# Optimization experiments

Measured on AMD Instinct MI355X. Metric: run time of the kernel, lower is better.

## Reference

```python
import jax, jax.numpy as jnp
import numpy as np

IN_FEATURES = 4096
OUT_FEATURES = 11008
BATCH = 256


def unpack_i4(q):
    # q: [K//2, N] packed bytes; row 2k = low nibble, row 2k+1 = high nibble
    low = q & 15
    high = (q >> 4) & 15
    # interleave -> [K, N]
    return jnp.stack([low, high], axis=1).reshape(q.shape[0] * 2, q.shape[1])


def setup_inputs() -> dict:
    key = jax.random.key(0)
    k1, k2, k3, k4 = jax.random.split(key, 4)
    x = jax.random.normal(k1, (BATCH, IN_FEATURES), dtype=jnp.float32)
    qweight = jax.random.randint(k2, (IN_FEATURES // 2, OUT_FEATURES), 0, 256, dtype=jnp.int32)
    scales = jax.random.uniform(k3, (OUT_FEATURES,), dtype=jnp.float32)
    zeroes = jax.random.normal(k4, (OUT_FEATURES,), dtype=jnp.float32)
    return {"x": x, "qweight": qweight, "scales": scales, "zeroes": zeroes}


def reference(x, qweight, scales, zeroes):
    # Dequantize: per-output-channel scale/zero over unpacked int4 weights
    w = scales[None, :] * unpack_i4(qweight).astype(jnp.float32) - zeroes[None, :]  # [K, N]
    return x @ w  # [B, N]
```

## Files before the change

### kernel.cpp

```cpp
#include <hip/hip_runtime.h>
#include <stdint.h>

#define K_DIM 4096
#define N_DIM 11008
#define M_DIM 256

typedef uint32_t u32;
using frag_ab = __attribute__((ext_vector_type(8))) short;
using frag_cd = __attribute__((ext_vector_type(4))) float;

typedef __attribute__((address_space(3))) const char lds_cc;

#define DSR128(dst, addr, off)                                       \
    asm volatile("ds_read_b128 %0, %1 offset:" #off                  \
                 : "=&v"(dst) : "v"(addr))
#define DSR32(dst, addr, off)                                        \
    asm volatile("ds_read_b32 %0, %1 offset:" #off                   \
                 : "=&v"(dst) : "v"(addr))

__device__ __forceinline__ u32 f2bf_rn(float f) {
    u32 u = __builtin_bit_cast(u32, f);
    return (u + 0x7FFFu + ((u >> 16) & 1u)) >> 16;
}
__device__ __forceinline__ float bf2f(u32 b) {
    return __builtin_bit_cast(float, b << 16);
}
__device__ __forceinline__ void gll16(const void* g, void* l) {
    __builtin_amdgcn_global_load_lds(
        (const __attribute__((address_space(1))) u32*)g,
        (__attribute__((address_space(3))) u32*)l, 16, 0, 0);
}

#define BFCVT(q) ((u32)((__mul24((int)(q), 0x4004) & 0x003C003C) | 0x42004200))

__global__ __launch_bounds__(256) void prep_kernel(const float* __restrict__ x,
                                                   ushort* __restrict__ xbf,
                                                   float* __restrict__ rowsum) {
    const int row = blockIdx.x;
    const int tid = threadIdx.x;
    const float* xr = x + (size_t)row * K_DIM;
    ushort* br = xbf + (size_t)row * K_DIM;
    float s = 0.0f;
#pragma unroll
    for (int p = 0; p < 4; ++p) {
        int i = p * 1024 + tid * 4;
        float4 v = *reinterpret_cast<const float4*>(xr + i);
        u32 b0 = f2bf_rn(v.x), b1 = f2bf_rn(v.y), b2 = f2bf_rn(v.z), b3 = f2bf_rn(v.w);
        uint2 o;
        o.x = b0 | (b1 << 16);
        o.y = b2 | (b3 << 16);
        *reinterpret_cast<uint2*>(br + i) = o;
        s += bf2f(b0) + bf2f(b1) + bf2f(b2) + bf2f(b3);
    }
#pragma unroll
    for (int off = 32; off > 0; off >>= 1) s += __shfl_down(s, off, 64);
    __shared__ float wsum[4];
    if ((tid & 63) == 0) wsum[tid >> 6] = s;
    __syncthreads();
    if (tid == 0) rowsum[row] = wsum[0] + wsum[1] + wsum[2] + wsum[3];
}

__global__ __launch_bounds__(512, 4) void gemm_kernel(const int* __restrict__ qw,
                                                      const float* __restrict__ scales,
                                                      const float* __restrict__ zeroes,
                                                      const ushort* __restrict__ xbf,
                                                      const float* __restrict__ rowsum,
                                                      float* __restrict__ out,
                                                      ushort* __restrict__ partial,
                                                      int split4) {
    __shared__ uint4 Alds[3][1024];
    __shared__ u32   Blds[3][2048];

    const u32* qwu = (const u32*)qw;
    const int tid  = threadIdx.x;
    const int lane = tid & 63;
    const int wid  = tid >> 6;
    const int l4   = lane & 15;
    const int c    = lane >> 4;

    const int orig = blockIdx.x;
    int nb, sp, NTt, kb;
    if (split4) {
        int wg = (orig & 7) * 43 + (orig >> 3);
        nb = wg >> 2; sp = wg & 3; NTt = 32; kb = sp * 32;
    } else {
        nb = orig; sp = 0; NTt = 128; kb = 0;
    }
    const int n0 = nb * 128;
    const int wm = wid >> 1;
    const int wn = wid & 1;

    const ushort* asrc[2];
#pragma unroll
    for (int j = 0; j < 2; ++j)
        asrc[j] = xbf + (size_t)((wid * 2 + j) * 16 + (lane >> 2)) * K_DIM +
                  8 * ((lane & 3) ^ ((lane >> 3) & 3));
    const u32* bsrc = qwu + (size_t)(wid * 2 + (lane >> 5)) * N_DIM + n0 +
                      (((lane & 31) * 4) ^ (((wid >> 1) & 1) << 4));

    const u32 aoff = (u32)((wm * 64 + l4) * 64 + ((c ^ ((l4 >> 1) & 3)) << 4));
    const u32 b0off = (u32)((c * 512 + wn * 64 + ((c & 1) << 4) + l4) * 4);
    const u32 b1off = (u32)((c * 512 + wn * 64 + ((1 ^ (c & 1)) << 4) + l4) * 4);

    frag_cd acc[4][4];
#pragma unroll
    for (int i = 0; i < 4; ++i)
#pragma unroll
        for (int j = 0; j < 4; ++j)
            acc[i][j] = (frag_cd){0.f, 0.f, 0.f, 0.f};

    auto stage = [&](int t, int buf) {
#pragma unroll
        for (int j = 0; j < 2; ++j)
            gll16(asrc[j] + (size_t)(kb + t) * 32, &Alds[buf][(wid * 2 + j) * 64]);
        gll16(bsrc + (size_t)(kb + t) * 16 * N_DIM, &Blds[buf][wid * 256]);
    };

    auto compute = [&](int buf) {
        lds_cc* Ab = (lds_cc*)&Alds[buf][0];
        lds_cc* Bb = (lds_cc*)&Blds[buf][0];
        frag_ab afr[4];
        DSR128(afr[0], Ab + aoff, 0);
        DSR128(afr[1], Ab + aoff, 1024);
        DSR128(afr[2], Ab + aoff, 2048);
        DSR128(afr[3], Ab + aoff, 3072);
        u32 bq[16];
        DSR32(bq[0],  Bb + b0off, 0);
        DSR32(bq[1],  Bb + b0off, 512);
        DSR32(bq[2],  Bb + b0off, 1024);
        DSR32(bq[3],  Bb + b0off, 1536);
        DSR32(bq[4],  Bb + b1off, 0);
        DSR32(bq[5],  Bb + b1off, 512);
        DSR32(bq[6],  Bb + b1off, 1024);
        DSR32(bq[7],  Bb + b1off, 1536);
        DSR32(bq[8],  Bb + b0off, 128);
        DSR32(bq[9],  Bb + b0off, 640);
        DSR32(bq[10], Bb + b0off, 1152);
        DSR32(bq[11], Bb + b0off, 1664);
        DSR32(bq[12], Bb + b1off, 128);
        DSR32(bq[13], Bb + b1off, 640);
        DSR32(bq[14], Bb + b1off, 1152);
        DSR32(bq[15], Bb + b1off, 1664);
        asm volatile("s_waitcnt lgkmcnt(0)" ::: "memory");
        __builtin_amdgcn_sched_barrier(0);
#pragma unroll
        for (int nf = 0; nf < 4; ++nf) {
            union { frag_ab f; u32 u[4]; } bb;
            bb.u[0] = BFCVT(bq[nf * 4 + 0]);
            bb.u[1] = BFCVT(bq[nf * 4 + 1]);
            bb.u[2] = BFCVT(bq[nf * 4 + 2]);
            bb.u[3] = BFCVT(bq[nf * 4 + 3]);
#pragma unroll
            for (int mf = 0; mf < 4; ++mf)
                acc[mf][nf] = __builtin_amdgcn_mfma_f32_16x16x32_bf16(
                    afr[mf], bb.f, acc[mf][nf], 0, 0, 0);
        }
    };

    stage(0, 0);
    stage(1, 1);

    int cur = 0;
    for (int t = 0; t < NTt; ++t) {
        int pbuf = cur + 2; if (pbuf >= 3) pbuf -= 3;
        if (t + 2 < NTt) {
            stage(t + 2, pbuf);
            asm volatile("s_waitcnt vmcnt(6)" ::: "memory");
        } else if (t + 1 < NTt) {
            asm volatile("s_waitcnt vmcnt(3)" ::: "memory");
        } else {
            asm volatile("s_waitcnt vmcnt(0)" ::: "memory");
        }
        __builtin_amdgcn_s_barrier();
        __builtin_amdgcn_sched_barrier(0);
        compute(cur);
        asm volatile("" ::: "memory");
        __builtin_amdgcn_s_barrier();
        ++cur; if (cur >= 3) cur -= 3;
    }

    float sc[4], zp[4];
#pragma unroll
    for (int nf = 0; nf < 4; ++nf) {
        int n = n0 + wn * 64 + nf * 16 + l4;
        sc[nf] = scales[n];
        zp[nf] = zeroes[n] + 32.0f * sc[nf];
    }
    if (sp == 0) {
        float rs[4][4];
#pragma unroll
        for (int mf = 0; mf < 4; ++mf)
#pragma unroll
            for (int j = 0; j < 4; ++j)
                rs[mf][j] = rowsum[wm * 64 + mf * 16 + c * 4 + j];
#pragma unroll
        for (int mf = 0; mf < 4; ++mf)
#pragma unroll
            for (int nf = 0; nf < 4; ++nf)
#pragma unroll
                for (int j = 0; j < 4; ++j) {
                    int m = wm * 64 + mf * 16 + c * 4 + j;
                    out[(size_t)m * N_DIM + n0 + wn * 64 + nf * 16 + l4] =
                        sc[nf] * acc[mf][nf][j] - zp[nf] * rs[mf][j];
                }
    } else {
        ushort* pb = partial + (size_t)(sp - 1) * M_DIM * N_DIM;
#pragma unroll
        for (int mf = 0; mf < 4; ++mf)
#pragma unroll
            for (int nf = 0; nf < 4; ++nf)
#pragma unroll
                for (int j = 0; j < 4; ++j) {
                    int m = wm * 64 + mf * 16 + c * 4 + j;
                    pb[(size_t)m * N_DIM + n0 + wn * 64 + nf * 16 + l4] =
                        (ushort)f2bf_rn(sc[nf] * acc[mf][nf][j]);
                }
    }
}

__global__ __launch_bounds__(256) void reduce_kernel(float* __restrict__ out,
                                                     const ushort* __restrict__ partial) {
    const size_t NTOT = (size_t)M_DIM * N_DIM;
    size_t i = ((size_t)blockIdx.x * 256 + threadIdx.x) * 4;
    float4 o = *reinterpret_cast<float4*>(out + i);
    ushort4 a = *reinterpret_cast<const ushort4*>(partial + i);
    ushort4 b = *reinterpret_cast<const ushort4*>(partial + NTOT + i);
    ushort4 d = *reinterpret_cast<const ushort4*>(partial + 2 * NTOT + i);
    o.x += bf2f(a.x) + bf2f(b.x) + bf2f(d.x);
    o.y += bf2f(a.y) + bf2f(b.y) + bf2f(d.y);
    o.z += bf2f(a.z) + bf2f(b.z) + bf2f(d.z);
    o.w += bf2f(a.w) + bf2f(b.w) + bf2f(d.w);
    *reinterpret_cast<float4*>(out + i) = o;
}

extern "C" void kernel_launch(void* const* d_in, const int* in_sizes, int n_in,
                              void* d_out, int out_size, void* d_ws, size_t ws_size,
                              hipStream_t stream) {
    const float* x      = (const float*)d_in[0];
    const int*   qw     = (const int*)d_in[1];
    const float* scales = (const float*)d_in[2];
    const float* zeroes = (const float*)d_in[3];
    float* out = (float*)d_out;

    const size_t XBF_BYTES = (size_t)M_DIM * K_DIM * 2;
    const size_t RS_OFF    = XBF_BYTES;
    const size_t P_OFF     = XBF_BYTES + 4096;
    const size_t P_BYTES   = (size_t)3 * M_DIM * N_DIM * 2;

    ushort* xbf    = (ushort*)d_ws;
    float*  rowsum = (float*)((char*)d_ws + RS_OFF);
    ushort* part   = (ushort*)((char*)d_ws + P_OFF);

    const bool split4 = ws_size >= P_OFF + P_BYTES;

    prep_kernel<<<M_DIM, 256, 0, stream>>>(x, xbf, rowsum);
    if (split4) {
        gemm_kernel<<<344, 512, 0, stream>>>(qw, scales, zeroes, xbf, rowsum,
                                             out, part, 1);
        reduce_kernel<<<(M_DIM * N_DIM) / (256 * 4), 256, 0, stream>>>(out, part);
    } else {
        gemm_kernel<<<86, 512, 0, stream>>>(qw, scales, zeroes, xbf, rowsum,
                                            out, nullptr, 0);
    }
}
```

Baseline: 53.01 us.

## Split GEMM tile into two M halves with 256-thread blocks

Each block now covers 128 rows of M instead of all 256 and runs with 256 threads, so twice as many blocks are launched (688 for split-K). The A/B staging is reworked so each wave loads more per stage, with the waitcnt values raised to match. A swizzle on the A layout is dropped. The goal is better occupancy and load balance across CUs. In exchange, each quantized weight tile is fetched and dequantized twice, once per M half, and the unswizzled LDS reads may hit bank conflicts.

New measurement: 50.67 us. 1.05x faster.

```diff
diff --git a/kernel.cpp b/kernel.cpp
--- a/kernel.cpp
+++ b/kernel.cpp
@@ -60,7 +60,7 @@
     if (tid == 0) rowsum[row] = wsum[0] + wsum[1] + wsum[2] + wsum[3];
 }
 
-__global__ __launch_bounds__(512, 4) void gemm_kernel(const int* __restrict__ qw,
+__global__ __launch_bounds__(256, 3) void gemm_kernel(const int* __restrict__ qw,
                                                       const float* __restrict__ scales,
                                                       const float* __restrict__ zeroes,
                                                       const ushort* __restrict__ xbf,
@@ -68,7 +68,7 @@
                                                       float* __restrict__ out,
                                                       ushort* __restrict__ partial,
                                                       int split4) {
-    __shared__ uint4 Alds[3][1024];
+    __shared__ uint4 Alds[3][512];
     __shared__ u32   Blds[3][2048];
 
     const u32* qwu = (const u32*)qw;
@@ -79,28 +79,32 @@
     const int c    = lane >> 4;
 
     const int orig = blockIdx.x;
-    int nb, sp, NTt, kb;
+    int nb, mb, sp, NTt;
     if (split4) {
-        int wg = (orig & 7) * 43 + (orig >> 3);
-        nb = wg >> 2; sp = wg & 3; NTt = 32; kb = sp * 32;
+        int wg = (orig & 7) * 86 + (orig >> 3);
+        nb = wg >> 3; sp = (wg >> 1) & 3; mb = wg & 1; NTt = 32;
     } else {
-        nb = orig; sp = 0; NTt = 128; kb = 0;
+        nb = orig >> 1; mb = orig & 1; sp = 0; NTt = 128;
     }
     const int n0 = nb * 128;
+    const int m0 = mb * 128;
     const int wm = wid >> 1;
     const int wn = wid & 1;
 
     const ushort* asrc[2];
 #pragma unroll
     for (int j = 0; j < 2; ++j)
-        asrc[j] = xbf + (size_t)((wid * 2 + j) * 16 + (lane >> 2)) * K_DIM +
-                  8 * ((lane & 3) ^ ((lane >> 3) & 3));
-    const u32* bsrc = qwu + (size_t)(wid * 2 + (lane >> 5)) * N_DIM + n0 +
-                      (((lane & 31) * 4) ^ (((wid >> 1) & 1) << 4));
-
-    const u32 aoff = (u32)((wm * 64 + l4) * 64 + ((c ^ ((l4 >> 1) & 3)) << 4));
-    const u32 b0off = (u32)((c * 512 + wn * 64 + ((c & 1) << 4) + l4) * 4);
-    const u32 b1off = (u32)((c * 512 + wn * 64 + ((1 ^ (c & 1)) << 4) + l4) * 4);
+        asrc[j] = xbf + (size_t)(m0 + j * 64 + wid * 16 + (lane >> 2)) * K_DIM +
+                  sp * 1024 + (lane & 3) * 8;
+    const u32* bsrc[2];
+#pragma unroll
+    for (int r = 0; r < 2; ++r)
+        bsrc[r] = qwu + (size_t)(sp * 512 + r * 8 + wid * 2 + (lane >> 5)) * N_DIM +
+                  n0 + 4 * ((lane & 31) ^ (((wid >> 1) & 1) << 2));
+
+    const u32 aoff  = (u32)((wm * 64 + l4) * 64 + c * 16);
+    const u32 b0off = (u32)((c * 4) * 512 + (wn * 64 + ((c & 1) << 4) + l4) * 4);
+    const u32 b1off = (u32)((c * 4) * 512 + (wn * 64 + ((1 ^ (c & 1)) << 4) + l4) * 4);
 
     frag_cd acc[4][4];
 #pragma unroll
@@ -112,8 +116,10 @@
     auto stage = [&](int t, int buf) {
 #pragma unroll
         for (int j = 0; j < 2; ++j)
-            gll16(asrc[j] + (size_t)(kb + t) * 32, &Alds[buf][(wid * 2 + j) * 64]);
-        gll16(bsrc + (size_t)(kb + t) * 16 * N_DIM, &Blds[buf][wid * 256]);
+            gll16(asrc[j] + (size_t)t * 32, &Alds[buf][j * 256 + wid * 64]);
+#pragma unroll
+        for (int r = 0; r < 2; ++r)
+            gll16(bsrc[r] + (size_t)t * 16 * N_DIM, &Blds[buf][r * 1024 + wid * 256]);
     };
 
     auto compute = [&](int buf) {
@@ -165,9 +171,9 @@
         int pbuf = cur + 2; if (pbuf >= 3) pbuf -= 3;
         if (t + 2 < NTt) {
             stage(t + 2, pbuf);
-            asm volatile("s_waitcnt vmcnt(6)" ::: "memory");
+            asm volatile("s_waitcnt vmcnt(8)" ::: "memory");
         } else if (t + 1 < NTt) {
-            asm volatile("s_waitcnt vmcnt(3)" ::: "memory");
+            asm volatile("s_waitcnt vmcnt(4)" ::: "memory");
         } else {
             asm volatile("s_waitcnt vmcnt(0)" ::: "memory");
         }
@@ -192,14 +198,14 @@
         for (int mf = 0; mf < 4; ++mf)
 #pragma unroll
             for (int j = 0; j < 4; ++j)
-                rs[mf][j] = rowsum[wm * 64 + mf * 16 + c * 4 + j];
+                rs[mf][j] = rowsum[m0 + wm * 64 + mf * 16 + c * 4 + j];
 #pragma unroll
         for (int mf = 0; mf < 4; ++mf)
 #pragma unroll
             for (int nf = 0; nf < 4; ++nf)
 #pragma unroll
                 for (int j = 0; j < 4; ++j) {
-                    int m = wm * 64 + mf * 16 + c * 4 + j;
+                    int m = m0 + wm * 64 + mf * 16 + c * 4 + j;
                     out[(size_t)m * N_DIM + n0 + wn * 64 + nf * 16 + l4] =
                         sc[nf] * acc[mf][nf][j] - zp[nf] * rs[mf][j];
                 }
@@ -211,7 +217,7 @@
             for (int nf = 0; nf < 4; ++nf)
 #pragma unroll
                 for (int j = 0; j < 4; ++j) {
-                    int m = wm * 64 + mf * 16 + c * 4 + j;
+                    int m = m0 + wm * 64 + mf * 16 + c * 4 + j;
                     pb[(size_t)m * N_DIM + n0 + wn * 64 + nf * 16 + l4] =
                         (ushort)f2bf_rn(sc[nf] * acc[mf][nf][j]);
                 }
@@ -255,11 +261,11 @@
 
     prep_kernel<<<M_DIM, 256, 0, stream>>>(x, xbf, rowsum);
     if (split4) {
-        gemm_kernel<<<344, 512, 0, stream>>>(qw, scales, zeroes, xbf, rowsum,
+        gemm_kernel<<<688, 256, 0, stream>>>(qw, scales, zeroes, xbf, rowsum,
                                              out, part, 1);
         reduce_kernel<<<(M_DIM * N_DIM) / (256 * 4), 256, 0, stream>>>(out, part);
     } else {
-        gemm_kernel<<<86, 512, 0, stream>>>(qw, scales, zeroes, xbf, rowsum,
-                                            out, nullptr, 0);
-    }
-}
+        gemm_kernel<<<172, 256, 0, stream>>>(qw, scales, zeroes, xbf, rowsum,
+                                             out, nullptr, 0);
+    }
+}
```
